# Kernel optimization log

Measured on AMD Instinct MI355X. Metric: run time of the kernel, lower is better.

Reference implementation:

```python
import jax, jax.numpy as jnp
import numpy as np

VOCAB, HID = 32000, 1024
SEQ, BATCH = 64, 32

def setup_inputs() -> dict:
    key = jax.random.key(0)
    ks = jax.random.split(key, 12)
    w = 0.1  # winit uniform(-winit, winit)
    u = lambda k, shape: jax.random.uniform(k, shape, jnp.float32, -w, w)
    return {
        "x": jax.random.randint(ks[0], (SEQ, BATCH), 0, VOCAB),
        "emb_W": u(ks[1], (VOCAB, HID)),
        "Wx0": u(ks[2], (4 * HID, HID)), "Wh0": u(ks[3], (4 * HID, HID)),
        "bx0": u(ks[4], (4 * HID,)), "bh0": u(ks[5], (4 * HID,)),
        "Wx1": u(ks[6], (4 * HID, HID)), "Wh1": u(ks[7], (4 * HID, HID)),
        "bx1": u(ks[8], (4 * HID,)), "bh1": u(ks[9], (4 * HID,)),
        "fc_W": u(ks[10], (VOCAB, HID)), "fc_b": u(ks[11], (VOCAB,)),
        "h0": jnp.zeros((BATCH, HID), jnp.float32),
        "c0": jnp.zeros((BATCH, HID), jnp.float32),
        "h1": jnp.zeros((BATCH, HID), jnp.float32),
        "c1": jnp.zeros((BATCH, HID), jnp.float32),
    }

def _lstm_layer(inp, h, c, Wx, Wh, bx, bh):
    # inp: [T, B, H]; h, c: [B, H]
    def step(carry, x_t):
        h, c = carry
        gx = x_t @ Wx.T + bx      # [B, 4H]
        gh = h @ Wh.T + bh        # [B, 4H]
        xi, xf, xo, xn = jnp.split(gx, 4, axis=1)
        hi, hf, ho, hn = jnp.split(gh, 4, axis=1)
        i = jax.nn.sigmoid(xi + hi)
        f = jax.nn.sigmoid(xf + hf)
        o = jax.nn.sigmoid(xo + ho)
        n = jnp.tanh(xn + hn)
        c = f * c + i * n
        h = o * jnp.tanh(c)
        return (h, c), h
    (h, c), ys = jax.lax.scan(step, (h, c), inp)
    return ys, h, c

def reference(x, emb_W, Wx0, Wh0, bx0, bh0, Wx1, Wh1, bx1, bh1,
              fc_W, fc_b, h0, c0, h1, c1):
    e = emb_W[x]                                   # [T, B, H] embedding gather
    y0, h0f, c0f = _lstm_layer(e, h0, c0, Wx0, Wh0, bx0, bh0)
    y1, h1f, c1f = _lstm_layer(y0, h1, c1, Wx1, Wh1, bx1, bh1)
    # Linear.forward flattens to [T*B, H] then projects to vocab (dropout=0)
    logits = y1.reshape(-1, y1.shape[-1]) @ fc_W.T + fc_b  # [T*B, V]
    return logits, h0f, c0f, h1f, c1f
```

## Files before the change

### kernel.cpp

```cpp
#include <hip/hip_runtime.h>
#include <hip/hip_bf16.h>
#include <stdint.h>

typedef __bf16 bf16x8 __attribute__((ext_vector_type(8)));
typedef float  f32x4  __attribute__((ext_vector_type(4)));

#define HID   1024
#define SEQT  64
#define BATCH 32
#define GATES 4096
#define ROWS  2048
#define VOCAB 32000
#define HSLAB (64 * 32 * 16)
#define AGT __HIP_MEMORY_SCOPE_AGENT

__device__ __forceinline__ unsigned short f2bf(float f) {
    union { float f; unsigned u; } v; v.f = f;
    unsigned u = v.u + 0x7FFFu + ((v.u >> 16) & 1u);
    return (unsigned short)(u >> 16);
}

__device__ __forceinline__ float sigm(float x) { return 1.f / (1.f + expf(-x)); }

__device__ __forceinline__ void gload_lds16(const void* g, void* l) {
    __builtin_amdgcn_global_load_lds(
        (const __attribute__((address_space(1))) unsigned int*)g,
        (__attribute__((address_space(3))) unsigned int*)l,
        16, 0, 0);
}

__device__ __forceinline__ ushort4 cvt4(float4 v) {
    ushort4 o;
    o.x = f2bf(v.x); o.y = f2bf(v.y); o.z = f2bf(v.z); o.w = f2bf(v.w);
    return o;
}

__global__ __launch_bounds__(256) void prologue_k(
    const int* __restrict__ x, const float* __restrict__ embW,
    unsigned short* __restrict__ eb,
    const float* __restrict__ Wx0, unsigned short* __restrict__ Wx0b,
    const float* __restrict__ h0, const float* __restrict__ h1,
    unsigned short* __restrict__ h0b, unsigned short* __restrict__ h1b,
    int* __restrict__ bar)
{
    const int bid = blockIdx.x, tid = threadIdx.x;
    const float4* src = (const float4*)(embW + (size_t)x[bid] * HID);
    ((ushort4*)(eb + (size_t)bid * HID))[tid] = cvt4(src[tid]);
    int base = bid * 512 + tid;
    ((ushort4*)Wx0b)[base]       = cvt4(((const float4*)Wx0)[base]);
    ((ushort4*)Wx0b)[base + 256] = cvt4(((const float4*)Wx0)[base + 256]);
    int i = bid * 256 + tid;
    if (i < 32768) {
        int blk = i >> 9, b = (i >> 4) & 31, w = i & 15;
        int col = blk * 16 + w;
        h0b[i] = f2bf(h0[b * HID + col]);
        h1b[i] = f2bf(h1[b * HID + col]);
        if (i < 8192) bar[i] = 0;
    }
}

__global__ __launch_bounds__(256) void gemm_bt(
    const unsigned short* __restrict__ A,
    const unsigned short* __restrict__ B,
    float* __restrict__ C,
    const float* __restrict__ bias0,
    const float* __restrict__ bias1,
    int M, int N, int K)
{
    __shared__ unsigned short As[128][32];
    __shared__ unsigned short Bs[128][32];
    const int tid  = threadIdx.x;
    const int lane = tid & 63;
    const int wr   = (tid >> 7) & 1;
    const int wc   = (tid >> 6) & 1;

    const int nmp = M >> 7, nnp = N >> 7;
    const int nwg = nmp * nnp, per = nwg >> 3;
    const int wid = (blockIdx.x & 7) * per + (blockIdx.x >> 3);
    const int bm  = (wid % nmp) << 7;
    const int bn  = (wid / nmp) << 7;

    const int lr   = lane & 15;
    const int lk   = (lane >> 4) * 8;

    f32x4 acc[4][4];
    #pragma unroll
    for (int m = 0; m < 4; ++m)
        #pragma unroll
        for (int n = 0; n < 4; ++n) acc[m][n] = 0.f;

    for (int kt = 0; kt < K; kt += 32) {
        __syncthreads();
        #pragma unroll
        for (int i = 0; i < 2; ++i) {
            int ch = tid + i * 256;
            int r = ch >> 2, c8 = (ch & 3) * 8;
            gload_lds16(A + (size_t)(bm + r) * K + kt + c8, (char*)&As[0][0] + ch * 16);
            gload_lds16(B + (size_t)(bn + r) * K + kt + c8, (char*)&Bs[0][0] + ch * 16);
        }
        __syncthreads();
        bf16x8 af[4], bfr[4];
        #pragma unroll
        for (int m = 0; m < 4; ++m)
            af[m] = *(const bf16x8*)&As[wr * 64 + m * 16 + lr][lk];
        #pragma unroll
        for (int n = 0; n < 4; ++n)
            bfr[n] = *(const bf16x8*)&Bs[wc * 64 + n * 16 + lr][lk];
        #pragma unroll
        for (int m = 0; m < 4; ++m)
            #pragma unroll
            for (int n = 0; n < 4; ++n)
                acc[m][n] = __builtin_amdgcn_mfma_f32_16x16x32_bf16(af[m], bfr[n], acc[m][n], 0, 0, 0);
    }

    const int row0 = bm + wr * 64, col0 = bn + wc * 64;
    #pragma unroll
    for (int n = 0; n < 4; ++n) {
        int col = col0 + n * 16 + lr;
        float badd = 0.f;
        if (bias0) badd += bias0[col];
        if (bias1) badd += bias1[col];
        #pragma unroll
        for (int m = 0; m < 4; ++m) {
            #pragma unroll
            for (int j = 0; j < 4; ++j) {
                int row = row0 + m * 16 + (lane >> 4) * 4 + j;
                C[(size_t)row * N + col] = acc[m][n][j] + badd;
            }
        }
    }
}

__global__ __launch_bounds__(256, 1) void lstm_fused_k(
    const float* __restrict__ Wh0f,
    const float* __restrict__ Wx1f,
    const float* __restrict__ Wh1f,
    const float* __restrict__ gx0,
    const float* __restrict__ bx1,
    const float* __restrict__ bh1,
    const unsigned short* __restrict__ h0b,
    const unsigned short* __restrict__ h1b,
    const float* __restrict__ c0i,
    const float* __restrict__ c1i,
    unsigned short* __restrict__ y0x,
    unsigned short* __restrict__ y1x,
    float* __restrict__ part,
    float* __restrict__ h0f, float* __restrict__ c0f,
    float* __restrict__ h1f, float* __restrict__ c1f,
    int* __restrict__ bar,
    const float* __restrict__ fcW,
    unsigned short* __restrict__ fcWb)
{
    const int tid = threadIdx.x;
    const int bid = blockIdx.x;

    if (bid >= 192) {
        int base = (bid - 192) * 256 + tid;
        const float4* f4 = (const float4*)fcW;
        uint4* o4 = (uint4*)fcWb;
        const int n8 = VOCAB * HID / 8;
        for (int i = base; i < n8; i += 16384) {
            float4 v0 = f4[2 * i], v1 = f4[2 * i + 1];
            uint4 o;
            o.x = (unsigned)f2bf(v0.x) | ((unsigned)f2bf(v0.y) << 16);
            o.y = (unsigned)f2bf(v0.z) | ((unsigned)f2bf(v0.w) << 16);
            o.z = (unsigned)f2bf(v1.x) | ((unsigned)f2bf(v1.y) << 16);
            o.w = (unsigned)f2bf(v1.z) | ((unsigned)f2bf(v1.w) << 16);
            o4[i] = o;
        }
        return;
    }

    __builtin_amdgcn_fence(__ATOMIC_ACQUIRE, "agent");

    __shared__ char smem[65536 + 8192];
    float* pre = (float*)(smem + 65536);
    const int lane = tid & 63;
    const int wave = tid >> 6;
    const int role = bid >> 6;
    const int wg   = bid & 63;
    const int lr   = lane & 15;
    const int lk8  = (lane >> 4) * 8;
    const int r0   = lr, r1 = 16 + lr;
    const int kby  = (lane >> 4) * 16;
    const int eb_  = tid >> 3;
    const int ecp  = (tid & 7) * 2;
    const int ecol = wg * 16 + ecp;

    bf16x8 wf[32];
    {
        const float* Wsrc = (role == 0) ? Wh0f : (role == 1) ? Wx1f : Wh1f;
        const float* p = Wsrc + (size_t)(wave * HID + wg * 16 + lr) * HID + lk8;
        #pragma unroll
        for (int kk = 0; kk < 32; ++kk) {
            float4 v0 = *(const float4*)(p + kk * 32);
            float4 v1 = *(const float4*)(p + kk * 32 + 4);
            union { bf16x8 v; unsigned short s[8]; } u;
            u.s[0] = f2bf(v0.x); u.s[1] = f2bf(v0.y);
            u.s[2] = f2bf(v0.z); u.s[3] = f2bf(v0.w);
            u.s[4] = f2bf(v1.x); u.s[5] = f2bf(v1.y);
            u.s[6] = f2bf(v1.z); u.s[7] = f2bf(v1.w);
            wf[kk] = u.v;
        }
        #pragma unroll
        for (int kk = 0; kk < 32; ++kk) asm volatile("" : "+v"(wf[kk]));
    }

    auto stage_g = [&](const unsigned short* src) {
        #pragma unroll
        for (int j = 0; j < 16; ++j) {
            int base = wave * 16384 + j * 1024;
            int d = base + lane * 16;
            int r = d >> 11;
            int cb = (d & 2047) ^ ((r & 7) << 4);
            int e0 = cb >> 1;
            int g = (((e0 >> 4) * 32 + r) * 16 + (e0 & 15)) * 2;
            gload_lds16((const char*)src + g, smem + base);
        }
    };
    auto mm = [&](f32x4& A0, f32x4& A1) {
        #pragma unroll
        for (int kk = 0; kk < 32; ++kk) {
            int k2 = kk * 64 + kby;
            bf16x8 x0 = *(const bf16x8*)(smem + r0 * 2048 + (k2 ^ ((r0 & 7) << 4)));
            bf16x8 x1 = *(const bf16x8*)(smem + r1 * 2048 + (k2 ^ ((r1 & 7) << 4)));
            A0 = __builtin_amdgcn_mfma_f32_16x16x32_bf16(x0, wf[kk], A0, 0, 0, 0);
            A1 = __builtin_amdgcn_mfma_f32_16x16x32_bf16(x1, wf[kk], A1, 0, 0, 0);
        }
    };
    auto spill = [&](const f32x4& a0, const f32x4& a1) {
        float* pg = pre + wave * 512;
        #pragma unroll
        for (int j = 0; j < 4; ++j) {
            pg[((lane >> 4) * 4 + j) * 16 + lr]        = a0[j];
            pg[((lane >> 4) * 4 + j + 16) * 16 + lr]   = a1[j];
        }
    };
    auto pollge = [&](int grp, int val) {
        for (;;) {
            int f = __hip_atomic_load(&bar[(grp * 64 + lane) * 32],
                                      __ATOMIC_RELAXED, AGT);
            if (__all(f >= val)) break;
            __builtin_amdgcn_s_sleep(1);
        }
    };

    if (role == 0) {
        float creg0, creg1;
        { float2 c2 = *(const float2*)&c0i[eb_ * HID + ecol]; creg0 = c2.x; creg1 = c2.y; }
        for (int t = 0; t < SEQT; ++t) {
            float2 gpre[4];
            const float* gxr = gx0 + (size_t)(t * BATCH + eb_) * GATES + ecol;
            #pragma unroll
            for (int g = 0; g < 4; ++g) gpre[g] = *(const float2*)(gxr + g * HID);
            if (t > 0) pollge(0, t);
            asm volatile("" ::: "memory");
            stage_g(t == 0 ? h0b : y0x + (size_t)(t - 1) * HSLAB);
            __syncthreads();
            f32x4 a0 = 0.f, a1 = 0.f;
            mm(a0, a1);
            spill(a0, a1);
            __syncthreads();
            float2 P[4];
            #pragma unroll
            for (int g = 0; g < 4; ++g) {
                float2 pr = *(const float2*)&pre[(g * 32 + eb_) * 16 + ecp];
                P[g].x = pr.x + gpre[g].x; P[g].y = pr.y + gpre[g].y;
            }
            float i0 = sigm(P[0].x), fg0 = sigm(P[1].x), o0 = sigm(P[2].x), n0 = tanhf(P[3].x);
            float i1 = sigm(P[0].y), fg1 = sigm(P[1].y), o1 = sigm(P[2].y), n1 = tanhf(P[3].y);
            float cn0 = fg0 * creg0 + i0 * n0, cn1 = fg1 * creg1 + i1 * n1;
            float hv0 = o0 * tanhf(cn0), hv1 = o1 * tanhf(cn1);
            creg0 = cn0; creg1 = cn1;
            unsigned pk = (unsigned)f2bf(hv0) | ((unsigned)f2bf(hv1) << 16);
            __hip_atomic_store(
                (unsigned*)&y0x[(size_t)t * HSLAB + (wg * 32 + eb_) * 16 + ecp],
                pk, __ATOMIC_RELAXED, AGT);
            if (t == SEQT - 1) {
                *(float2*)&h0f[eb_ * HID + ecol] = make_float2(hv0, hv1);
                *(float2*)&c0f[eb_ * HID + ecol] = make_float2(cn0, cn1);
            }
            __syncthreads();
            if (tid == 0)
                __hip_atomic_store(&bar[wg * 32], t + 1, __ATOMIC_RELAXED, AGT);
        }
    } else if (role == 1) {
        for (int t = 0; t < SEQT; ++t) {
            pollge(0, t + 1);
            asm volatile("" ::: "memory");
            stage_g(y0x + (size_t)t * HSLAB);
            __syncthreads();
            f32x4 a0 = 0.f, a1 = 0.f;
            mm(a0, a1);
            {
                float* pb = part + (((size_t)(t * 4 + wave) * 64 + wg) * 32) * 16;
                int brow = (lane >> 4) * 4;
                #pragma unroll
                for (int j = 0; j < 4; ++j) {
                    __hip_atomic_store(pb + (brow + j) * 16 + lr,      a0[j],
                                       __ATOMIC_RELAXED, AGT);
                    __hip_atomic_store(pb + (brow + j + 16) * 16 + lr, a1[j],
                                       __ATOMIC_RELAXED, AGT);
                }
            }
            __syncthreads();
            if (tid == 0)
                __hip_atomic_store(&bar[(64 + wg) * 32], t + 1, __ATOMIC_RELAXED, AGT);
        }
    } else {
        float creg0, creg1;
        { float2 c2 = *(const float2*)&c1i[eb_ * HID + ecol]; creg0 = c2.x; creg1 = c2.y; }
        float2 b1r[4];
        #pragma unroll
        for (int g = 0; g < 4; ++g) {
            float2 a = *(const float2*)&bx1[g * HID + ecol];
            float2 b = *(const float2*)&bh1[g * HID + ecol];
            b1r[g].x = a.x + b.x; b1r[g].y = a.y + b.y;
        }
        for (int t = 0; t < SEQT; ++t) {
            pollge(1, t + 1);
            if (t > 0) pollge(2, t);
            asm volatile("" ::: "memory");
            stage_g(t == 0 ? h1b : y1x + (size_t)(t - 1) * HSLAB);
            __syncthreads();
            f32x4 a0 = 0.f, a1 = 0.f;
            mm(a0, a1);
            spill(a0, a1);
            __syncthreads();
            float2 P[4];
            #pragma unroll
            for (int g = 0; g < 4; ++g) {
                float2 pr = *(const float2*)&pre[(g * 32 + eb_) * 16 + ecp];
                float2 px = *(const float2*)(part +
                    ((((size_t)(t * 4 + g) * 64 + wg) * 32 + eb_) * 16 + ecp));
                P[g].x = pr.x + px.x + b1r[g].x;
                P[g].y = pr.y + px.y + b1r[g].y;
            }
            float i0 = sigm(P[0].x), fg0 = sigm(P[1].x), o0 = sigm(P[2].x), n0 = tanhf(P[3].x);
            float i1 = sigm(P[0].y), fg1 = sigm(P[1].y), o1 = sigm(P[2].y), n1 = tanhf(P[3].y);
            float cn0 = fg0 * creg0 + i0 * n0, cn1 = fg1 * creg1 + i1 * n1;
            float hv0 = o0 * tanhf(cn0), hv1 = o1 * tanhf(cn1);
            creg0 = cn0; creg1 = cn1;
            unsigned pk = (unsigned)f2bf(hv0) | ((unsigned)f2bf(hv1) << 16);
            __hip_atomic_store(
                (unsigned*)&y1x[(size_t)t * HSLAB + (wg * 32 + eb_) * 16 + ecp],
                pk, __ATOMIC_RELAXED, AGT);
            if (t == SEQT - 1) {
                *(float2*)&h1f[eb_ * HID + ecol] = make_float2(hv0, hv1);
                *(float2*)&c1f[eb_ * HID + ecol] = make_float2(cn0, cn1);
            }
            __syncthreads();
            if (tid == 0)
                __hip_atomic_store(&bar[(128 + wg) * 32], t + 1, __ATOMIC_RELAXED, AGT);
        }
    }
}

__global__ __launch_bounds__(512) void fc_k(
    const unsigned short* __restrict__ y1x,
    const unsigned short* __restrict__ fcWb,
    const float* __restrict__ fcb,
    float* __restrict__ logits)
{
    __shared__ unsigned short As[256 * 64];
    __shared__ unsigned short Bs[128 * 64];
    const int tid  = threadIdx.x;
    const int lane = tid & 63;
    const int wave = tid >> 6;
    const int wr   = wave >> 1;
    const int wc   = wave & 1;
    const int lr   = lane & 15;
    const int lk2  = (lane >> 4) * 16;

    const int per = 2000 >> 3;
    const int wid = ((int)blockIdx.x & 7) * per + ((int)blockIdx.x >> 3);
    const int bm  = (wid & 7) << 8;
    const int bn  = (wid >> 3) << 7;

    f32x4 acc[4][4];
    #pragma unroll
    for (int m = 0; m < 4; ++m)
        #pragma unroll
        for (int n = 0; n < 4; ++n) acc[m][n] = 0.f;

    for (int kt = 0; kt < HID; kt += 64) {
        __syncthreads();
        #pragma unroll
        for (int i = 0; i < 4; ++i) {
            int ch = tid + i * 512;
            int row = ch >> 3, ck = ch & 7;
            int R = bm + row;
            int e = kt + ((ck ^ (row & 7)) << 3);
            const char* asrc = (const char*)y1x +
                ((((size_t)(R >> 5) * 64 + (e >> 4)) * 32 + (R & 31)) * 16 + (e & 15)) * 2;
            gload_lds16(asrc, (char*)As + ch * 16);
        }
        #pragma unroll
        for (int i = 0; i < 2; ++i) {
            int ch = tid + i * 512;
            int row = ch >> 3, ck = ch & 7;
            int e = kt + ((ck ^ (row & 7)) << 3);
            gload_lds16(fcWb + (size_t)(bn + row) * HID + e, (char*)Bs + ch * 16);
        }
        __syncthreads();
        #pragma unroll
        for (int kh = 0; kh < 2; ++kh) {
            bf16x8 af[4], bfr[4];
            #pragma unroll
            for (int m = 0; m < 4; ++m) {
                int row = wr * 64 + m * 16 + lr;
                af[m] = *(const bf16x8*)((char*)As + row * 128 +
                         ((kh * 64 + lk2) ^ ((row & 7) << 4)));
            }
            #pragma unroll
            for (int n = 0; n < 4; ++n) {
                int row = wc * 64 + n * 16 + lr;
                bfr[n] = *(const bf16x8*)((char*)Bs + row * 128 +
                         ((kh * 64 + lk2) ^ ((row & 7) << 4)));
            }
            #pragma unroll
            for (int m = 0; m < 4; ++m)
                #pragma unroll
                for (int n = 0; n < 4; ++n)
                    acc[m][n] = __builtin_amdgcn_mfma_f32_16x16x32_bf16(
                        af[m], bfr[n], acc[m][n], 0, 0, 0);
        }
    }

    const int row0 = bm + wr * 64, col0 = bn + wc * 64;
    #pragma unroll
    for (int n = 0; n < 4; ++n) {
        int col = col0 + n * 16 + lr;
        float badd = fcb[col];
        #pragma unroll
        for (int m = 0; m < 4; ++m) {
            #pragma unroll
            for (int j = 0; j < 4; ++j) {
                int row = row0 + m * 16 + (lane >> 4) * 4 + j;
                logits[(size_t)row * VOCAB + col] = acc[m][n][j] + badd;
            }
        }
    }
}

extern "C" void kernel_launch(void* const* d_in, const int* in_sizes, int n_in,
                              void* d_out, int out_size, void* d_ws, size_t ws_size,
                              hipStream_t stream) {
    const int*   x    = (const int*)d_in[0];
    const float* embW = (const float*)d_in[1];
    const float* Wx0  = (const float*)d_in[2];
    const float* Wh0  = (const float*)d_in[3];
    const float* bx0  = (const float*)d_in[4];
    const float* bh0  = (const float*)d_in[5];
    const float* Wx1  = (const float*)d_in[6];
    const float* Wh1  = (const float*)d_in[7];
    const float* bx1  = (const float*)d_in[8];
    const float* bh1  = (const float*)d_in[9];
    const float* fcW  = (const float*)d_in[10];
    const float* fcb  = (const float*)d_in[11];
    const float* h0   = (const float*)d_in[12];
    const float* c0   = (const float*)d_in[13];
    const float* h1   = (const float*)d_in[14];
    const float* c1   = (const float*)d_in[15];

    char* ws = (char*)d_ws;
    size_t off = 0;
    auto alloc = [&](size_t bytes) {
        char* p = ws + off;
        off += (bytes + 255) & ~(size_t)255;
        return p;
    };
    unsigned short* eb    = (unsigned short*)alloc((size_t)ROWS * HID * 2);
    unsigned short* Wx0b  = (unsigned short*)alloc((size_t)GATES * HID * 2);
    unsigned short* fcWb  = (unsigned short*)alloc((size_t)VOCAB * HID * 2);
    float*          gx0   = (float*)alloc((size_t)ROWS * GATES * 4);
    float*          part  = (float*)alloc((size_t)SEQT * 4 * 64 * 32 * 16 * 4);
    unsigned short* y0x   = (unsigned short*)alloc((size_t)SEQT * HSLAB * 2);
    unsigned short* y1x   = (unsigned short*)alloc((size_t)SEQT * HSLAB * 2);
    unsigned short* h0b   = (unsigned short*)alloc((size_t)BATCH * HID * 2);
    unsigned short* h1b   = (unsigned short*)alloc((size_t)BATCH * HID * 2);
    int*            bar   = (int*)alloc((size_t)256 * 32 * 4);
    (void)ws_size; (void)in_sizes; (void)n_in; (void)out_size;

    float* logits = (float*)d_out;
    float* h0f = logits + (size_t)ROWS * VOCAB;
    float* c0f = h0f + BATCH * HID;
    float* h1f = c0f + BATCH * HID;
    float* c1f = h1f + BATCH * HID;

    prologue_k<<<ROWS, 256, 0, stream>>>(x, embW, eb, Wx0, Wx0b,
                                         h0, h1, h0b, h1b, bar);
    gemm_bt<<<(ROWS / 128) * (GATES / 128), 256, 0, stream>>>(
        eb, Wx0b, gx0, bx0, bh0, ROWS, GATES, HID);
    lstm_fused_k<<<256, 256, 0, stream>>>(Wh0, Wx1, Wh1, gx0, bx1, bh1,
                                          h0b, h1b, c0, c1, y0x, y1x, part,
                                          h0f, c0f, h1f, c1f, bar, fcW, fcWb);
    fc_k<<<2000, 512, 0, stream>>>(y1x, fcWb, fcb, logits);
}
```

Baseline: 563.7 us.

## Replace flag barriers with NaN-sentinel data polling in fused LSTM kernel

Removes the per-step flag array and its wait/signal barriers between the three LSTM roles. The prologue now fills the y0/y1 hidden-state buffers and the partial-sum buffer with a NaN bf16 sentinel, and consumers spin on atomic loads of the data itself until no sentinel words remain, then write the values into LDS. This drops a syncthreads and a flag round trip from each recurrent step, but it costs extra prologue writes, swaps the async global-to-LDS loads for register loads plus LDS stores, and relies on real outputs never matching the sentinel bit pattern.

```diff
diff --git a/kernel.cpp b/kernel.cpp
--- a/kernel.cpp
+++ b/kernel.cpp
@@ -12,6 +12,7 @@
 #define ROWS  2048
 #define VOCAB 32000
 #define HSLAB (64 * 32 * 16)
+#define SENTW 0x7FC07FC0u
 #define AGT __HIP_MEMORY_SCOPE_AGENT
 
 __device__ __forceinline__ unsigned short f2bf(float f) {
@@ -33,6 +34,13 @@
     ushort4 o;
     o.x = f2bf(v.x); o.y = f2bf(v.y); o.z = f2bf(v.z); o.w = f2bf(v.w);
     return o;
+}
+
+__device__ __forceinline__ unsigned long long aload(const void* p) {
+    return __hip_atomic_load((const unsigned long long*)p, __ATOMIC_RELAXED, AGT);
+}
+__device__ __forceinline__ int okw(unsigned long long q) {
+    return ((unsigned)q != SENTW) & ((unsigned)(q >> 32) != SENTW);
 }
 
 __global__ __launch_bounds__(256) void prologue_k(
@@ -41,7 +49,8 @@
     const float* __restrict__ Wx0, unsigned short* __restrict__ Wx0b,
     const float* __restrict__ h0, const float* __restrict__ h1,
     unsigned short* __restrict__ h0b, unsigned short* __restrict__ h1b,
-    int* __restrict__ bar)
+    uint4* __restrict__ y0x4, uint4* __restrict__ y1x4,
+    uint4* __restrict__ part4)
 {
     const int bid = blockIdx.x, tid = threadIdx.x;
     const float4* src = (const float4*)(embW + (size_t)x[bid] * HID);
@@ -55,8 +64,14 @@
         int col = blk * 16 + w;
         h0b[i] = f2bf(h0[b * HID + col]);
         h1b[i] = f2bf(h1[b * HID + col]);
-        if (i < 8192) bar[i] = 0;
-    }
+    }
+    uint4 s4; s4.x = s4.y = s4.z = s4.w = SENTW;
+    if (i < 262144) y0x4[i] = s4;
+    else            y1x4[i - 262144] = s4;
+    part4[i]           = s4;
+    part4[i + 524288]  = s4;
+    part4[i + 1048576] = s4;
+    part4[i + 1572864] = s4;
 }
 
 __global__ __launch_bounds__(256) void gemm_bt(
@@ -147,7 +162,6 @@
     float* __restrict__ part,
     float* __restrict__ h0f, float* __restrict__ c0f,
     float* __restrict__ h1f, float* __restrict__ c1f,
-    int* __restrict__ bar,
     const float* __restrict__ fcW,
     unsigned short* __restrict__ fcWb)
 {
@@ -206,16 +220,35 @@
         for (int kk = 0; kk < 32; ++kk) asm volatile("" : "+v"(wf[kk]));
     }
 
-    auto stage_g = [&](const unsigned short* src) {
+    int goff[16];
+    #pragma unroll
+    for (int j = 0; j < 16; ++j) {
+        int base = wave * 16384 + j * 1024;
+        int d = base + lane * 16;
+        int r = d >> 11;
+        int cb = (d & 2047) ^ ((r & 7) << 4);
+        int e0 = cb >> 1;
+        goff[j] = (((e0 >> 4) * 32 + r) * 16 + (e0 & 15)) * 2;
+    }
+
+    auto stage_v = [&](const unsigned short* src) {
+        const char* s = (const char*)src;
+        unsigned long long v0[16], v1[16];
         #pragma unroll
         for (int j = 0; j < 16; ++j) {
-            int base = wave * 16384 + j * 1024;
-            int d = base + lane * 16;
-            int r = d >> 11;
-            int cb = (d & 2047) ^ ((r & 7) << 4);
-            int e0 = cb >> 1;
-            int g = (((e0 >> 4) * 32 + r) * 16 + (e0 & 15)) * 2;
-            gload_lds16((const char*)src + g, smem + base);
+            v0[j] = aload(s + goff[j]);
+            v1[j] = aload(s + goff[j] + 8);
+        }
+        #pragma unroll
+        for (int j = 0; j < 16; ++j) {
+            for (;;) {
+                int ok = okw(v0[j]) & okw(v1[j]);
+                if (__all(ok)) break;
+                if (!okw(v0[j])) v0[j] = aload(s + goff[j]);
+                if (!okw(v1[j])) v1[j] = aload(s + goff[j] + 8);
+            }
+            ulonglong2 u; u.x = v0[j]; u.y = v1[j];
+            *(ulonglong2*)(smem + wave * 16384 + j * 1024 + lane * 16) = u;
         }
     };
     auto mm = [&](f32x4& A0, f32x4& A1) {
@@ -236,14 +269,6 @@
             pg[((lane >> 4) * 4 + j + 16) * 16 + lr]   = a1[j];
         }
     };
-    auto pollge = [&](int grp, int val) {
-        for (;;) {
-            int f = __hip_atomic_load(&bar[(grp * 64 + lane) * 32],
-                                      __ATOMIC_RELAXED, AGT);
-            if (__all(f >= val)) break;
-            __builtin_amdgcn_s_sleep(1);
-        }
-    };
 
     if (role == 0) {
         float creg0, creg1;
@@ -253,9 +278,7 @@
             const float* gxr = gx0 + (size_t)(t * BATCH + eb_) * GATES + ecol;
             #pragma unroll
             for (int g = 0; g < 4; ++g) gpre[g] = *(const float2*)(gxr + g * HID);
-            if (t > 0) pollge(0, t);
-            asm volatile("" ::: "memory");
-            stage_g(t == 0 ? h0b : y0x + (size_t)(t - 1) * HSLAB);
+            stage_v(t == 0 ? h0b : y0x + (size_t)(t - 1) * HSLAB);
             __syncthreads();
             f32x4 a0 = 0.f, a1 = 0.f;
             mm(a0, a1);
@@ -280,18 +303,14 @@
                 *(float2*)&h0f[eb_ * HID + ecol] = make_float2(hv0, hv1);
                 *(float2*)&c0f[eb_ * HID + ecol] = make_float2(cn0, cn1);
             }
-            __syncthreads();
-            if (tid == 0)
-                __hip_atomic_store(&bar[wg * 32], t + 1, __ATOMIC_RELAXED, AGT);
         }
     } else if (role == 1) {
         for (int t = 0; t < SEQT; ++t) {
-            pollge(0, t + 1);
-            asm volatile("" ::: "memory");
-            stage_g(y0x + (size_t)t * HSLAB);
+            stage_v(y0x + (size_t)t * HSLAB);
             __syncthreads();
             f32x4 a0 = 0.f, a1 = 0.f;
             mm(a0, a1);
+            __syncthreads();
             {
                 float* pb = part + (((size_t)(t * 4 + wave) * 64 + wg) * 32) * 16;
                 int brow = (lane >> 4) * 4;
@@ -303,9 +322,6 @@
                                        __ATOMIC_RELAXED, AGT);
                 }
             }
-            __syncthreads();
-            if (tid == 0)
-                __hip_atomic_store(&bar[(64 + wg) * 32], t + 1, __ATOMIC_RELAXED, AGT);
         }
     } else {
         float creg0, creg1;
@@ -318,10 +334,7 @@
             b1r[g].x = a.x + b.x; b1r[g].y = a.y + b.y;
         }
         for (int t = 0; t < SEQT; ++t) {
-            pollge(1, t + 1);
-            if (t > 0) pollge(2, t);
-            asm volatile("" ::: "memory");
-            stage_g(t == 0 ? h1b : y1x + (size_t)(t - 1) * HSLAB);
+            stage_v(t == 0 ? h1b : y1x + (size_t)(t - 1) * HSLAB);
             __syncthreads();
             f32x4 a0 = 0.f, a1 = 0.f;
             mm(a0, a1);
@@ -331,10 +344,16 @@
             #pragma unroll
             for (int g = 0; g < 4; ++g) {
                 float2 pr = *(const float2*)&pre[(g * 32 + eb_) * 16 + ecp];
-                float2 px = *(const float2*)(part +
-                    ((((size_t)(t * 4 + g) * 64 + wg) * 32 + eb_) * 16 + ecp));
-                P[g].x = pr.x + px.x + b1r[g].x;
-                P[g].y = pr.y + px.y + b1r[g].y;
+                const float* pxp = part +
+                    ((((size_t)(t * 4 + g) * 64 + wg) * 32 + eb_) * 16 + ecp);
+                unsigned long long q;
+                for (;;) {
+                    q = aload(pxp);
+                    if (__all(okw(q))) break;
+                }
+                union { unsigned long long u; float2 f; } pc; pc.u = q;
+                P[g].x = pr.x + pc.f.x + b1r[g].x;
+                P[g].y = pr.y + pc.f.y + b1r[g].y;
             }
             float i0 = sigm(P[0].x), fg0 = sigm(P[1].x), o0 = sigm(P[2].x), n0 = tanhf(P[3].x);
             float i1 = sigm(P[0].y), fg1 = sigm(P[1].y), o1 = sigm(P[2].y), n1 = tanhf(P[3].y);
@@ -349,9 +368,6 @@
                 *(float2*)&h1f[eb_ * HID + ecol] = make_float2(hv0, hv1);
                 *(float2*)&c1f[eb_ * HID + ecol] = make_float2(cn0, cn1);
             }
-            __syncthreads();
-            if (tid == 0)
-                __hip_atomic_store(&bar[(128 + wg) * 32], t + 1, __ATOMIC_RELAXED, AGT);
         }
     }
 }
@@ -479,7 +495,6 @@
     unsigned short* y1x   = (unsigned short*)alloc((size_t)SEQT * HSLAB * 2);
     unsigned short* h0b   = (unsigned short*)alloc((size_t)BATCH * HID * 2);
     unsigned short* h1b   = (unsigned short*)alloc((size_t)BATCH * HID * 2);
-    int*            bar   = (int*)alloc((size_t)256 * 32 * 4);
     (void)ws_size; (void)in_sizes; (void)n_in; (void)out_size;
 
     float* logits = (float*)d_out;
@@ -489,11 +504,12 @@
     float* c1f = h1f + BATCH * HID;
 
     prologue_k<<<ROWS, 256, 0, stream>>>(x, embW, eb, Wx0, Wx0b,
-                                         h0, h1, h0b, h1b, bar);
+                                         h0, h1, h0b, h1b,
+                                         (uint4*)y0x, (uint4*)y1x, (uint4*)part);
     gemm_bt<<<(ROWS / 128) * (GATES / 128), 256, 0, stream>>>(
         eb, Wx0b, gx0, bx0, bh0, ROWS, GATES, HID);
     lstm_fused_k<<<256, 256, 0, stream>>>(Wh0, Wx1, Wh1, gx0, bx1, bh1,
                                           h0b, h1b, c0, c1, y0x, y1x, part,
-                                          h0f, c0f, h1f, c1f, bar, fcW, fcWb);
+                                          h0f, c0f, h1f, c1f, fcW, fcWb);
     fc_k<<<2000, 512, 0, stream>>>(y1x, fcWb, fcb, logits);
 }
```

Result: slower. 997.3 us (+76.9%).

## Overlap first vocab panels of FC projection with LSTM recurrence in idle blocks

Applied to the files above, without the earlier changes.

The 64 extra blocks of the fused LSTM kernel used to only convert fc_W to bf16. Now each also computes one 128-column vocab panel of the logits, processing 128-row chunks of y1 as soon as the layer-1 barrier shows the needed timesteps are done. The standalone fc_k launch shrinks to cover only the remaining columns (from 8192 onward). This hides part of the projection under the latency-bound recurrence, but the extra blocks compete for CUs and memory bandwidth with the LSTM blocks and rely on the barrier counters to track y1 progress correctly.

```diff
diff --git a/kernel.cpp b/kernel.cpp
--- a/kernel.cpp
+++ b/kernel.cpp
@@ -149,33 +149,116 @@
     float* __restrict__ h1f, float* __restrict__ c1f,
     int* __restrict__ bar,
     const float* __restrict__ fcW,
-    unsigned short* __restrict__ fcWb)
+    unsigned short* __restrict__ fcWb,
+    const float* __restrict__ fcb,
+    float* __restrict__ logits)
 {
-    const int tid = threadIdx.x;
-    const int bid = blockIdx.x;
-
-    if (bid >= 192) {
-        int base = (bid - 192) * 256 + tid;
-        const float4* f4 = (const float4*)fcW;
-        uint4* o4 = (uint4*)fcWb;
-        const int n8 = VOCAB * HID / 8;
-        for (int i = base; i < n8; i += 16384) {
-            float4 v0 = f4[2 * i], v1 = f4[2 * i + 1];
-            uint4 o;
-            o.x = (unsigned)f2bf(v0.x) | ((unsigned)f2bf(v0.y) << 16);
-            o.y = (unsigned)f2bf(v0.z) | ((unsigned)f2bf(v0.w) << 16);
-            o.z = (unsigned)f2bf(v1.x) | ((unsigned)f2bf(v1.y) << 16);
-            o.w = (unsigned)f2bf(v1.z) | ((unsigned)f2bf(v1.w) << 16);
-            o4[i] = o;
-        }
-        return;
-    }
+    const int tid  = threadIdx.x;
+    const int bid  = blockIdx.x;
+    const int lane = tid & 63;
 
     __builtin_amdgcn_fence(__ATOMIC_ACQUIRE, "agent");
 
     __shared__ char smem[65536 + 8192];
     float* pre = (float*)(smem + 65536);
-    const int lane = tid & 63;
+
+    auto pollge = [&](int grp, int val) {
+        for (;;) {
+            int f = __hip_atomic_load(&bar[(grp * 64 + lane) * 32],
+                                      __ATOMIC_RELAXED, AGT);
+            if (__all(f >= val)) break;
+            __builtin_amdgcn_s_sleep(1);
+        }
+    };
+
+    if (bid >= 192) {
+        const int p = bid - 192;
+        auto cvtpanel = [&](int q) {
+            const float4* f4 = (const float4*)(fcW + (size_t)q * 128 * HID);
+            uint4* o4 = (uint4*)(fcWb + (size_t)q * 128 * HID);
+            for (int i = tid; i < 128 * HID / 8; i += 256) {
+                float4 v0 = f4[2 * i], v1 = f4[2 * i + 1];
+                uint4 o;
+                o.x = (unsigned)f2bf(v0.x) | ((unsigned)f2bf(v0.y) << 16);
+                o.y = (unsigned)f2bf(v0.z) | ((unsigned)f2bf(v0.w) << 16);
+                o.z = (unsigned)f2bf(v1.x) | ((unsigned)f2bf(v1.y) << 16);
+                o.w = (unsigned)f2bf(v1.z) | ((unsigned)f2bf(v1.w) << 16);
+                o4[i] = o;
+            }
+        };
+        cvtpanel(p);
+        for (int q = 64 + p; q < 250; q += 64) cvtpanel(q);
+        __syncthreads();
+
+        const int wr = (tid >> 7) & 1, wc = (tid >> 6) & 1;
+        const int lr = lane & 15;
+        const int lk2 = (lane >> 4) * 16;
+        unsigned short* As = (unsigned short*)smem;
+        unsigned short* Bs = (unsigned short*)(smem + 16384);
+        for (int m = 0; m < 16; ++m) {
+            pollge(2, 4 * m + 4);
+            asm volatile("" ::: "memory");
+            f32x4 acc[4][4];
+            #pragma unroll
+            for (int mi = 0; mi < 4; ++mi)
+                #pragma unroll
+                for (int ni = 0; ni < 4; ++ni) acc[mi][ni] = 0.f;
+            for (int kt = 0; kt < HID; kt += 64) {
+                __syncthreads();
+                #pragma unroll
+                for (int i = 0; i < 4; ++i) {
+                    int ch = tid + i * 256;
+                    int row = ch >> 3, ck = ch & 7;
+                    int R = m * 128 + row;
+                    int e = kt + ((ck ^ (row & 7)) << 3);
+                    const char* asrc = (const char*)y1x +
+                        ((((size_t)(R >> 5) * 64 + (e >> 4)) * 32 + (R & 31)) * 16 + (e & 15)) * 2;
+                    gload_lds16(asrc, (char*)As + ch * 16);
+                    gload_lds16(fcWb + (size_t)(p * 128 + row) * HID + e,
+                                (char*)Bs + ch * 16);
+                }
+                __syncthreads();
+                #pragma unroll
+                for (int kh = 0; kh < 2; ++kh) {
+                    bf16x8 af[4], bfr[4];
+                    #pragma unroll
+                    for (int mi = 0; mi < 4; ++mi) {
+                        int row = wr * 64 + mi * 16 + lr;
+                        af[mi] = *(const bf16x8*)((char*)As + row * 128 +
+                                 ((kh * 64 + lk2) ^ ((row & 7) << 4)));
+                    }
+                    #pragma unroll
+                    for (int ni = 0; ni < 4; ++ni) {
+                        int row = wc * 64 + ni * 16 + lr;
+                        bfr[ni] = *(const bf16x8*)((char*)Bs + row * 128 +
+                                  ((kh * 64 + lk2) ^ ((row & 7) << 4)));
+                    }
+                    #pragma unroll
+                    for (int mi = 0; mi < 4; ++mi)
+                        #pragma unroll
+                        for (int ni = 0; ni < 4; ++ni)
+                            acc[mi][ni] = __builtin_amdgcn_mfma_f32_16x16x32_bf16(
+                                af[mi], bfr[ni], acc[mi][ni], 0, 0, 0);
+                }
+            }
+            const int row0 = m * 128 + wr * 64, col0 = p * 128 + wc * 64;
+            #pragma unroll
+            for (int ni = 0; ni < 4; ++ni) {
+                int col = col0 + ni * 16 + lr;
+                float badd = fcb[col];
+                #pragma unroll
+                for (int mi = 0; mi < 4; ++mi) {
+                    #pragma unroll
+                    for (int j = 0; j < 4; ++j) {
+                        int row = row0 + mi * 16 + (lane >> 4) * 4 + j;
+                        logits[(size_t)row * VOCAB + col] = acc[mi][ni][j] + badd;
+                    }
+                }
+            }
+        }
+        return;
+    }
+
     const int wave = tid >> 6;
     const int role = bid >> 6;
     const int wg   = bid & 63;
@@ -234,14 +317,6 @@
         for (int j = 0; j < 4; ++j) {
             pg[((lane >> 4) * 4 + j) * 16 + lr]        = a0[j];
             pg[((lane >> 4) * 4 + j + 16) * 16 + lr]   = a1[j];
-        }
-    };
-    auto pollge = [&](int grp, int val) {
-        for (;;) {
-            int f = __hip_atomic_load(&bar[(grp * 64 + lane) * 32],
-                                      __ATOMIC_RELAXED, AGT);
-            if (__all(f >= val)) break;
-            __builtin_amdgcn_s_sleep(1);
         }
     };
 
@@ -372,10 +447,10 @@
     const int lr   = lane & 15;
     const int lk2  = (lane >> 4) * 16;
 
-    const int per = 2000 >> 3;
+    const int per = 1488 >> 3;
     const int wid = ((int)blockIdx.x & 7) * per + ((int)blockIdx.x >> 3);
     const int bm  = (wid & 7) << 8;
-    const int bn  = (wid >> 3) << 7;
+    const int bn  = ((wid >> 3) + 64) << 7;
 
     f32x4 acc[4][4];
     #pragma unroll
@@ -494,6 +569,7 @@
         eb, Wx0b, gx0, bx0, bh0, ROWS, GATES, HID);
     lstm_fused_k<<<256, 256, 0, stream>>>(Wh0, Wx1, Wh1, gx0, bx1, bh1,
                                           h0b, h1b, c0, c1, y0x, y1x, part,
-                                          h0f, c0f, h1f, c1f, bar, fcW, fcWb);
-    fc_k<<<2000, 512, 0, stream>>>(y1x, fcWb, fcb, logits);
-}
+                                          h0f, c0f, h1f, c1f, bar, fcW, fcWb,
+                                          fcb, logits);
+    fc_k<<<1488, 512, 0, stream>>>(y1x, fcWb, fcb, logits);
+}
```

Result: slower. 619.1 us (+9.8%).
